# Optimization experiments

Measured on AMD Instinct MI355X. Metric: run time of the kernel, lower is better.

The kernel has to match this reference:

```python
import jax, jax.numpy as jnp
import numpy as np

N_NODES = 100000
N_EDGES = 1600000
D_IN = 64
D_OUT = 64


def setup_inputs() -> dict:
    key = jax.random.key(0)
    k1, k2, k3, k4 = jax.random.split(key, 4)
    feat = jax.random.normal(k1, (N_NODES, D_IN), dtype=jnp.float32)
    edge_src = jax.random.randint(k2, (N_EDGES,), 0, N_NODES, dtype=jnp.int64)
    edge_dst = jax.random.randint(k3, (N_EDGES,), 0, N_NODES, dtype=jnp.int64)
    # xavier_uniform with gain for relu (sqrt(2)) on [out, in] Linear weight
    gain = float(np.sqrt(2.0))
    limit = gain * float(np.sqrt(6.0 / (D_IN + D_OUT)))
    fc_weight = jax.random.uniform(k4, (D_OUT, D_IN), dtype=jnp.float32,
                                   minval=-limit, maxval=limit)
    return {"feat": feat, "edge_src": edge_src, "edge_dst": edge_dst,
            "fc_weight": fc_weight}


def reference(feat, edge_src, edge_dst, fc_weight):
    # SDDMM: edge score a_e = <h_src, h_dst>  (fn.u_dot_v)
    h_src = feat[edge_src]                      # [E, d]
    h_dst = feat[edge_dst]                      # [E, d]
    a = jnp.sum(h_src * h_dst, axis=-1, keepdims=True)  # [E, 1]
    # SpMM: neigh[v] = sum_{(u->v)} h_u * a_e  (u_mul_e + sum)
    m = h_src * a                               # [E, d]
    neigh = jax.ops.segment_sum(m, edge_dst, num_segments=feat.shape[0])  # [N, d]
    # Linear without bias: y = neigh @ W.T
    return neigh @ fc_weight.T
```

## Files before the change

### kernel.cpp

```cpp
#include <hip/hip_runtime.h>

#define N_NODES 100000
#define N_EDGES 1600000
#define D 64
#define NB 782
#define CAP 3072
#define EPB 8192
#define NPART ((N_EDGES + EPB - 1) / EPB)
#define RSH 14

typedef unsigned short ushort_t;
typedef unsigned int uint_t;

__device__ __forceinline__ ushort_t f2bf(float f) {
    uint_t u = __float_as_uint(f);
    u += 0x7FFF + ((u >> 16) & 1);
    return (ushort_t)(u >> 16);
}

__global__ __launch_bounds__(256) void repack_init(const float* __restrict__ feat,
                                                   ushort_t* __restrict__ featb,
                                                   int* __restrict__ gcur) {
    const int tid = blockIdx.x * 256 + threadIdx.x;
    if (tid < NB) gcur[tid] = tid * CAP;
    const int base = tid * 16;
    if (base >= N_NODES * D) return;
    const float4* f4 = (const float4*)(feat + base);
    ushort4* o4 = (ushort4*)(featb + base);
#pragma unroll
    for (int j = 0; j < 4; ++j) {
        const float4 v = f4[j];
        o4[j] = make_ushort4(f2bf(v.x), f2bf(v.y), f2bf(v.z), f2bf(v.w));
    }
}

__global__ __launch_bounds__(1024) void partition(const int* __restrict__ esrc,
                                                  const int* __restrict__ edst,
                                                  int* __restrict__ gcur,
                                                  int* __restrict__ slab) {
    __shared__ int stage[EPB];
    __shared__ ushort_t bkt16[EPB];
    __shared__ int cnt[NB];
    __shared__ int cur[NB];
    __shared__ int gb[NB];
    __shared__ int s[1024];
    const int t = threadIdx.x;
    const int base = blockIdx.x * EPB;
    const int n = min(EPB, N_EDGES - base);

    if (t < NB) cnt[t] = 0;
    __syncthreads();
    for (int i = t; i < n; i += 1024)
        atomicAdd(&cnt[edst[base + i] >> 7], 1);
    __syncthreads();
    const int v = (t < NB) ? cnt[t] : 0;
    s[t] = v;
    __syncthreads();
    for (int off = 1; off < 1024; off <<= 1) {
        const int x = (t >= off) ? s[t - off] : 0;
        __syncthreads();
        s[t] += x;
        __syncthreads();
    }
    if (t < NB) {
        const int excl = s[t] - v;
        cur[t] = excl;
        gb[t] = (v ? atomicAdd(&gcur[t], v) : 0) - excl;
    }
    __syncthreads();
    for (int i = t; i < n; i += 1024) {
        const int d = edst[base + i];
        const int bkt = d >> 7;
        const int pos = atomicAdd(&cur[bkt], 1);
        stage[pos] = ((d & 127) << 17) | esrc[base + i];
        bkt16[pos] = (ushort_t)bkt;
    }
    __syncthreads();
    for (int i = t; i < n; i += 1024) {
        const int bkt = bkt16[i];
        const int gp = gb[bkt] + i;
        if (gp < (bkt + 1) * CAP)
            slab[gp] = stage[i];
    }
}

template<int CTRL>
__device__ __forceinline__ float fadd_dpp(float x) {
    const int r = __builtin_amdgcn_update_dpp(0, __float_as_int(x), CTRL, 0xF, 0xF, true);
    return x + __int_as_float(r);
}
__device__ __forceinline__ float red8(float p) {
    p = fadd_dpp<0xB1>(p);
    p = fadd_dpp<0x4E>(p);
    p = fadd_dpp<0x141>(p);
    return p;
}

__device__ __forceinline__ float cvt_dot(const uint4 u, const float* __restrict__ h,
                                         float* __restrict__ g) {
    g[0] = __uint_as_float(u.x << 16); g[1] = __uint_as_float(u.x & 0xFFFF0000u);
    g[2] = __uint_as_float(u.y << 16); g[3] = __uint_as_float(u.y & 0xFFFF0000u);
    g[4] = __uint_as_float(u.z << 16); g[5] = __uint_as_float(u.z & 0xFFFF0000u);
    g[6] = __uint_as_float(u.w << 16); g[7] = __uint_as_float(u.w & 0xFFFF0000u);
    float p = 0.f;
#pragma unroll
    for (int k = 0; k < 8; ++k) p += g[k] * h[k];
    return p;
}

__global__ __launch_bounds__(512) void fused_spmm(const float4* __restrict__ feat4,
                                                  const uint4* __restrict__ featb4,
                                                  const int* __restrict__ slab,
                                                  const int* __restrict__ gcur,
                                                  float4* __restrict__ neigh4) {
    __shared__ int seA[CAP];
    __shared__ int seB[CAP];
    __shared__ int cnt[1024];
    __shared__ int cur[1024];
    __shared__ int rowoff[129];
    __shared__ int s[512];
    const int t = threadIdx.x;
    const int b = blockIdx.x;
    const int nbase = b << 7;
    const int nb_nodes = min(128, N_NODES - nbase);
    const int sbase = b * CAP;
    const int ne = min(gcur[b] - sbase, CAP);

    for (int i = t; i < ne; i += 512) seA[i] = slab[sbase + i];
    cnt[t] = 0; cnt[t + 512] = 0;
    __syncthreads();
    for (int i = t; i < ne; i += 512) {
        const int pk = seA[i];
        atomicAdd(&cnt[((pk >> 17) << 3) | ((pk & 0x1FFFF) >> RSH)], 1);
    }
    __syncthreads();
    const int v0 = cnt[2 * t], v1 = cnt[2 * t + 1];
    const int sum = v0 + v1;
    s[t] = sum;
    __syncthreads();
    for (int off = 1; off < 512; off <<= 1) {
        const int x = (t >= off) ? s[t - off] : 0;
        __syncthreads();
        s[t] += x;
        __syncthreads();
    }
    const int excl = s[t] - sum;
    cur[2 * t] = excl;
    cur[2 * t + 1] = excl + v0;
    __syncthreads();
    if (t < 128) rowoff[t] = cur[t << 3];
    if (t == 0) rowoff[128] = ne;
    __syncthreads();
    for (int i = t; i < ne; i += 512) {
        const int pk = seA[i];
        const int key = ((pk >> 17) << 3) | ((pk & 0x1FFFF) >> RSH);
        const int pos = atomicAdd(&cur[key], 1);
        seB[pos] = pk & 0x1FFFF;
    }
    __syncthreads();

    const int slot = t >> 3;
    const int l = t & 7;
#pragma unroll
    for (int ln0 = 0; ln0 < 128; ln0 += 64) {
        const int ln = ln0 + slot;
        if (ln >= nb_nodes) continue;
        const int nidx = nbase + ln;
        float h[8];
        {
            const float4 ha = feat4[nidx * 16 + 2 * l];
            const float4 hb = feat4[nidx * 16 + 2 * l + 1];
            h[0] = ha.x; h[1] = ha.y; h[2] = ha.z; h[3] = ha.w;
            h[4] = hb.x; h[5] = hb.y; h[6] = hb.z; h[7] = hb.w;
        }
        float acc[8];
#pragma unroll
        for (int k = 0; k < 8; ++k) acc[k] = 0.f;

        int e = rowoff[ln];
        const int e1 = rowoff[ln + 1];
        for (; e + 3 < e1; e += 4) {
            const int s0 = seB[e], s1 = seB[e + 1], s2 = seB[e + 2], s3 = seB[e + 3];
            const uint4 u0 = featb4[s0 * 8 + l];
            const uint4 u1 = featb4[s1 * 8 + l];
            const uint4 u2 = featb4[s2 * 8 + l];
            const uint4 u3 = featb4[s3 * 8 + l];
            float g0[8], g1[8], g2[8], g3[8];
            float p0 = cvt_dot(u0, h, g0);
            float p1 = cvt_dot(u1, h, g1);
            float p2 = cvt_dot(u2, h, g2);
            float p3 = cvt_dot(u3, h, g3);
            p0 = red8(p0); p1 = red8(p1); p2 = red8(p2); p3 = red8(p3);
#pragma unroll
            for (int k = 0; k < 8; ++k)
                acc[k] += g0[k] * p0 + g1[k] * p1 + g2[k] * p2 + g3[k] * p3;
        }
        for (; e < e1; ++e) {
            const uint4 u0 = featb4[seB[e] * 8 + l];
            float g0[8];
            float p0 = red8(cvt_dot(u0, h, g0));
#pragma unroll
            for (int k = 0; k < 8; ++k) acc[k] += g0[k] * p0;
        }
        neigh4[nidx * 16 + 2 * l]     = make_float4(acc[0], acc[1], acc[2], acc[3]);
        neigh4[nidx * 16 + 2 * l + 1] = make_float4(acc[4], acc[5], acc[6], acc[7]);
    }
}

__global__ __launch_bounds__(256) void gemm_inplace(float* __restrict__ out,
                                                    const float* __restrict__ W) {
    __shared__ float WT[64][68];
    __shared__ float nT[64][132];
    const int t = threadIdx.x;

    const float4* W4 = (const float4*)W;
#pragma unroll
    for (int j = 0; j < 4; ++j) {
        const int f = t + j * 256;
        const int o = f >> 4;
        const int i4 = (f & 15) * 4;
        const float4 w = W4[f];
        WT[i4 + 0][o] = w.x;
        WT[i4 + 1][o] = w.y;
        WT[i4 + 2][o] = w.z;
        WT[i4 + 3][o] = w.w;
    }

    const int base = blockIdx.x * 128;
    const int rows = min(128, N_NODES - base);
    const float4* O4 = (const float4*)(out + (long)base * D);
#pragma unroll
    for (int j = 0; j < 8; ++j) {
        const int f = t + j * 256;
        const int r = f >> 4;
        const int i4 = (f & 15) * 4;
        if (r < rows) {
            const float4 x = O4[f];
            nT[i4 + 0][r] = x.x;
            nT[i4 + 1][r] = x.y;
            nT[i4 + 2][r] = x.z;
            nT[i4 + 3][r] = x.w;
        }
    }
    __syncthreads();

    const int c4 = (t & 15) * 4;
    const int r0 = (t >> 4) * 8;
    float acc[8][4];
#pragma unroll
    for (int r = 0; r < 8; ++r)
#pragma unroll
        for (int c = 0; c < 4; ++c) acc[r][c] = 0.f;

    for (int i = 0; i < 64; ++i) {
        const float4 w = *(const float4*)&WT[i][c4];
        const float4 ra = *(const float4*)&nT[i][r0];
        const float4 rb = *(const float4*)&nT[i][r0 + 4];
        const float wv[4] = {w.x, w.y, w.z, w.w};
        const float rv[8] = {ra.x, ra.y, ra.z, ra.w, rb.x, rb.y, rb.z, rb.w};
#pragma unroll
        for (int r = 0; r < 8; ++r)
#pragma unroll
            for (int c = 0; c < 4; ++c) acc[r][c] += rv[r] * wv[c];
    }

#pragma unroll
    for (int r = 0; r < 8; ++r) {
        const int rr = r0 + r;
        if (rr < rows)
            *(float4*)&out[(long)(base + rr) * D + c4] =
                make_float4(acc[r][0], acc[r][1], acc[r][2], acc[r][3]);
    }
}

extern "C" void kernel_launch(void* const* d_in, const int* in_sizes, int n_in,
                              void* d_out, int out_size, void* d_ws, size_t ws_size,
                              hipStream_t stream) {
    const float* feat = (const float*)d_in[0];
    const int*   esrc = (const int*)d_in[1];
    const int*   edst = (const int*)d_in[2];
    const float* W    = (const float*)d_in[3];
    float* out = (float*)d_out;

    char* ws = (char*)d_ws;
    ushort_t* featb = (ushort_t*)(ws);
    int* slab = (int*)(ws + 12800000);
    int* gcur = (int*)(ws + 12800000 + (size_t)NB * CAP * 4);

    repack_init<<<(N_NODES * D / 16 + 255) / 256, 256, 0, stream>>>(feat, featb, gcur);
    partition<<<NPART, 1024, 0, stream>>>(esrc, edst, gcur, slab);
    fused_spmm<<<NB, 512, 0, stream>>>((const float4*)feat, (const uint4*)featb,
                                       slab, gcur, (float4*)out);
    gemm_inplace<<<(N_NODES + 127) / 128, 256, 0, stream>>>(out, W);
}
```

Measured before the change: 170.2 us.

## Fuse SpMM with output GEMM and balance node degrees across thread slots

Merges the separate linear-projection kernel into the aggregation kernel. The aggregated neighbor sums now go to shared memory, and the 64x64 weight multiply runs in the same block, so the intermediate no longer makes a round trip through global memory and one launch is dropped. It also sorts nodes by degree and pairs light nodes with heavy ones per thread slot to even out per-lane work. The cost is a serial O(128) rank computation per node, extra shared memory reuse that requires careful aliasing, and a smaller GEMM tile per thread.

```diff
diff --git a/kernel.cpp b/kernel.cpp
--- a/kernel.cpp
+++ b/kernel.cpp
@@ -108,17 +108,73 @@
     return p;
 }
 
-__global__ __launch_bounds__(512) void fused_spmm(const float4* __restrict__ feat4,
-                                                  const uint4* __restrict__ featb4,
-                                                  const int* __restrict__ slab,
-                                                  const int* __restrict__ gcur,
-                                                  float4* __restrict__ neigh4) {
-    __shared__ int seA[CAP];
-    __shared__ int seB[CAP];
-    __shared__ int cnt[1024];
-    __shared__ int cur[1024];
-    __shared__ int rowoff[129];
-    __shared__ int s[512];
+#define SMEM_BYTES 51200
+#define OFF_SEB    12288
+#define OFF_CNT    24576
+#define OFF_CUR    28672
+#define OFF_S      32768
+#define OFF_ROW    34816
+#define OFF_DEG    35332
+#define OFF_PERM   35844
+#define OFF_WT     33792
+
+#define EDGE_ROUND(ACC, LN)                                                    \
+    if ((LN) < nb_nodes) {                                                     \
+        float h[8];                                                            \
+        {                                                                      \
+            const int nidx = nbase + (LN);                                     \
+            const float4 ha = feat4[nidx * 16 + 2 * l];                        \
+            const float4 hb = feat4[nidx * 16 + 2 * l + 1];                    \
+            h[0] = ha.x; h[1] = ha.y; h[2] = ha.z; h[3] = ha.w;                \
+            h[4] = hb.x; h[5] = hb.y; h[6] = hb.z; h[7] = hb.w;                \
+        }                                                                      \
+        int e = rowoff[(LN)];                                                  \
+        const int e1 = rowoff[(LN) + 1];                                       \
+        for (; e + 3 < e1; e += 4) {                                           \
+            const int s0 = seB[e], s1 = seB[e + 1];                            \
+            const int s2 = seB[e + 2], s3 = seB[e + 3];                        \
+            const uint4 u0 = featb4[s0 * 8 + l];                               \
+            const uint4 u1 = featb4[s1 * 8 + l];                               \
+            const uint4 u2 = featb4[s2 * 8 + l];                               \
+            const uint4 u3 = featb4[s3 * 8 + l];                               \
+            float g0[8], g1[8], g2[8], g3[8];                                  \
+            float p0 = cvt_dot(u0, h, g0);                                     \
+            float p1 = cvt_dot(u1, h, g1);                                     \
+            float p2 = cvt_dot(u2, h, g2);                                     \
+            float p3 = cvt_dot(u3, h, g3);                                     \
+            p0 = red8(p0); p1 = red8(p1); p2 = red8(p2); p3 = red8(p3);        \
+            _Pragma("unroll")                                                  \
+            for (int k = 0; k < 8; ++k)                                        \
+                ACC[k] += g0[k] * p0 + g1[k] * p1 + g2[k] * p2 + g3[k] * p3;   \
+        }                                                                      \
+        for (; e < e1; ++e) {                                                  \
+            const uint4 u0 = featb4[seB[e] * 8 + l];                           \
+            float g0[8];                                                       \
+            float p0 = red8(cvt_dot(u0, h, g0));                               \
+            _Pragma("unroll")                                                  \
+            for (int k = 0; k < 8; ++k) ACC[k] += g0[k] * p0;                  \
+        }                                                                      \
+    }
+
+__global__ __launch_bounds__(512, 6) void fused_spmm_gemm(
+        const float4* __restrict__ feat4,
+        const uint4* __restrict__ featb4,
+        const int* __restrict__ slab,
+        const int* __restrict__ gcur,
+        const float* __restrict__ W,
+        float4* __restrict__ out4) {
+    __shared__ __align__(16) char smem[SMEM_BYTES];
+    int* seA    = (int*)(smem);
+    int* seB    = (int*)(smem + OFF_SEB);
+    int* cnt    = (int*)(smem + OFF_CNT);
+    int* cur    = (int*)(smem + OFF_CUR);
+    int* s      = (int*)(smem + OFF_S);
+    int* rowoff = (int*)(smem + OFF_ROW);
+    int* degs   = (int*)(smem + OFF_DEG);
+    int* perm   = (int*)(smem + OFF_PERM);
+    float (*nT)[132] = (float(*)[132])(smem);
+    float (*WT)[68]  = (float(*)[68])(smem + OFF_WT);
+
     const int t = threadIdx.x;
     const int b = blockIdx.x;
     const int nbase = b << 7;
@@ -151,6 +207,7 @@
     if (t < 128) rowoff[t] = cur[t << 3];
     if (t == 0) rowoff[128] = ne;
     __syncthreads();
+    if (t < 128) degs[t] = rowoff[t + 1] - rowoff[t];
     for (int i = t; i < ne; i += 512) {
         const int pk = seA[i];
         const int key = ((pk >> 17) << 3) | ((pk & 0x1FFFF) >> RSH);
@@ -158,118 +215,73 @@
         seB[pos] = pk & 0x1FFFF;
     }
     __syncthreads();
+    if (t < 128) {
+        const int d = degs[t];
+        int pos = 0;
+        for (int j = 0; j < 128; ++j) {
+            const int dj = degs[j];
+            pos += (dj < d) || (dj == d && j < t);
+        }
+        perm[pos] = t;
+    }
+    __syncthreads();
 
     const int slot = t >> 3;
     const int l = t & 7;
-#pragma unroll
-    for (int ln0 = 0; ln0 < 128; ln0 += 64) {
-        const int ln = ln0 + slot;
-        if (ln >= nb_nodes) continue;
-        const int nidx = nbase + ln;
-        float h[8];
-        {
-            const float4 ha = feat4[nidx * 16 + 2 * l];
-            const float4 hb = feat4[nidx * 16 + 2 * l + 1];
-            h[0] = ha.x; h[1] = ha.y; h[2] = ha.z; h[3] = ha.w;
-            h[4] = hb.x; h[5] = hb.y; h[6] = hb.z; h[7] = hb.w;
+    const int ln0 = perm[slot];
+    const int ln1 = perm[127 - slot];
+    float acc0[8], acc1[8];
+#pragma unroll
+    for (int k = 0; k < 8; ++k) { acc0[k] = 0.f; acc1[k] = 0.f; }
+    EDGE_ROUND(acc0, ln0)
+    EDGE_ROUND(acc1, ln1)
+    __syncthreads();
+
+#pragma unroll
+    for (int k = 0; k < 8; ++k) nT[8 * l + k][ln0] = acc0[k];
+#pragma unroll
+    for (int k = 0; k < 8; ++k) nT[8 * l + k][ln1] = acc1[k];
+    {
+        const float4* W4 = (const float4*)W;
+#pragma unroll
+        for (int j = 0; j < 2; ++j) {
+            const int f = t + j * 512;
+            const int o = f >> 4;
+            const int i4 = (f & 15) * 4;
+            const float4 w = W4[f];
+            WT[i4 + 0][o] = w.x;
+            WT[i4 + 1][o] = w.y;
+            WT[i4 + 2][o] = w.z;
+            WT[i4 + 3][o] = w.w;
         }
-        float acc[8];
-#pragma unroll
-        for (int k = 0; k < 8; ++k) acc[k] = 0.f;
-
-        int e = rowoff[ln];
-        const int e1 = rowoff[ln + 1];
-        for (; e + 3 < e1; e += 4) {
-            const int s0 = seB[e], s1 = seB[e + 1], s2 = seB[e + 2], s3 = seB[e + 3];
-            const uint4 u0 = featb4[s0 * 8 + l];
-            const uint4 u1 = featb4[s1 * 8 + l];
-            const uint4 u2 = featb4[s2 * 8 + l];
-            const uint4 u3 = featb4[s3 * 8 + l];
-            float g0[8], g1[8], g2[8], g3[8];
-            float p0 = cvt_dot(u0, h, g0);
-            float p1 = cvt_dot(u1, h, g1);
-            float p2 = cvt_dot(u2, h, g2);
-            float p3 = cvt_dot(u3, h, g3);
-            p0 = red8(p0); p1 = red8(p1); p2 = red8(p2); p3 = red8(p3);
-#pragma unroll
-            for (int k = 0; k < 8; ++k)
-                acc[k] += g0[k] * p0 + g1[k] * p1 + g2[k] * p2 + g3[k] * p3;
-        }
-        for (; e < e1; ++e) {
-            const uint4 u0 = featb4[seB[e] * 8 + l];
-            float g0[8];
-            float p0 = red8(cvt_dot(u0, h, g0));
-#pragma unroll
-            for (int k = 0; k < 8; ++k) acc[k] += g0[k] * p0;
-        }
-        neigh4[nidx * 16 + 2 * l]     = make_float4(acc[0], acc[1], acc[2], acc[3]);
-        neigh4[nidx * 16 + 2 * l + 1] = make_float4(acc[4], acc[5], acc[6], acc[7]);
-    }
-}
-
-__global__ __launch_bounds__(256) void gemm_inplace(float* __restrict__ out,
-                                                    const float* __restrict__ W) {
-    __shared__ float WT[64][68];
-    __shared__ float nT[64][132];
-    const int t = threadIdx.x;
-
-    const float4* W4 = (const float4*)W;
-#pragma unroll
-    for (int j = 0; j < 4; ++j) {
-        const int f = t + j * 256;
-        const int o = f >> 4;
-        const int i4 = (f & 15) * 4;
-        const float4 w = W4[f];
-        WT[i4 + 0][o] = w.x;
-        WT[i4 + 1][o] = w.y;
-        WT[i4 + 2][o] = w.z;
-        WT[i4 + 3][o] = w.w;
-    }
-
-    const int base = blockIdx.x * 128;
-    const int rows = min(128, N_NODES - base);
-    const float4* O4 = (const float4*)(out + (long)base * D);
-#pragma unroll
-    for (int j = 0; j < 8; ++j) {
-        const int f = t + j * 256;
-        const int r = f >> 4;
-        const int i4 = (f & 15) * 4;
-        if (r < rows) {
-            const float4 x = O4[f];
-            nT[i4 + 0][r] = x.x;
-            nT[i4 + 1][r] = x.y;
-            nT[i4 + 2][r] = x.z;
-            nT[i4 + 3][r] = x.w;
-        }
     }
     __syncthreads();
 
     const int c4 = (t & 15) * 4;
-    const int r0 = (t >> 4) * 8;
-    float acc[8][4];
-#pragma unroll
-    for (int r = 0; r < 8; ++r)
-#pragma unroll
-        for (int c = 0; c < 4; ++c) acc[r][c] = 0.f;
+    const int r0 = (t >> 4) * 4;
+    float a4[4][4];
+#pragma unroll
+    for (int r = 0; r < 4; ++r)
+#pragma unroll
+        for (int c = 0; c < 4; ++c) a4[r][c] = 0.f;
 
     for (int i = 0; i < 64; ++i) {
         const float4 w = *(const float4*)&WT[i][c4];
-        const float4 ra = *(const float4*)&nT[i][r0];
-        const float4 rb = *(const float4*)&nT[i][r0 + 4];
+        const float4 rv = *(const float4*)&nT[i][r0];
         const float wv[4] = {w.x, w.y, w.z, w.w};
-        const float rv[8] = {ra.x, ra.y, ra.z, ra.w, rb.x, rb.y, rb.z, rb.w};
-#pragma unroll
-        for (int r = 0; r < 8; ++r)
-#pragma unroll
-            for (int c = 0; c < 4; ++c) acc[r][c] += rv[r] * wv[c];
-    }
-
-#pragma unroll
-    for (int r = 0; r < 8; ++r) {
+        const float rr[4] = {rv.x, rv.y, rv.z, rv.w};
+#pragma unroll
+        for (int r = 0; r < 4; ++r)
+#pragma unroll
+            for (int c = 0; c < 4; ++c) a4[r][c] += rr[r] * wv[c];
+    }
+
+#pragma unroll
+    for (int r = 0; r < 4; ++r) {
         const int rr = r0 + r;
-        if (rr < rows)
-            *(float4*)&out[(long)(base + rr) * D + c4] =
-                make_float4(acc[r][0], acc[r][1], acc[r][2], acc[r][3]);
+        if (rr < nb_nodes)
+            out4[(long)(nbase + rr) * 16 + (t & 15)] =
+                make_float4(a4[r][0], a4[r][1], a4[r][2], a4[r][3]);
     }
 }
 
@@ -289,7 +301,6 @@
 
     repack_init<<<(N_NODES * D / 16 + 255) / 256, 256, 0, stream>>>(feat, featb, gcur);
     partition<<<NPART, 1024, 0, stream>>>(esrc, edst, gcur, slab);
-    fused_spmm<<<NB, 512, 0, stream>>>((const float4*)feat, (const uint4*)featb,
-                                       slab, gcur, (float4*)out);
-    gemm_inplace<<<(N_NODES + 127) / 128, 256, 0, stream>>>(out, W);
-}
+    fused_spmm_gemm<<<NB, 512, 0, stream>>>((const float4*)feat, (const uint4*)featb,
+                                            slab, gcur, W, (float4*)out);
+}
```

Result: slower. 191.5 us (+12.5%).
